# Optimization experiments

Measured on AMD Instinct MI355X. Metric: run time of the kernel, lower is better.

The kernel has to match this reference:

```python
import jax, jax.numpy as jnp
import numpy as np

N_NODES = 100000
N_EDGES = 3200000
NFEAT, NHID, NCLASS = 512, 256, 40


def spmm(edge_src, edge_dst, edge_w, h):
    # sparse adjacency @ h via gather + weighted segment-sum over destination nodes
    msgs = h[edge_src] * edge_w[:, None]          # [E, d]
    return jax.ops.segment_sum(msgs, edge_dst, num_segments=N_NODES)


def gcn_layer(h, W, b, edge_src, edge_dst, edge_w):
    support = h @ W                                # [N, d_out]
    return spmm(edge_src, edge_dst, edge_w, support) + b


def setup_inputs() -> dict:
    key = jax.random.key(0)
    ks = jax.random.split(key, 16)
    def w(k, shape, fan_in):
        return jax.random.normal(k, shape, dtype=jnp.float32) / np.sqrt(fan_in)
    inp = {
        'x': jax.random.normal(ks[0], (N_NODES, NFEAT), dtype=jnp.float32),
        'W1': w(ks[1], (NFEAT, NHID), NFEAT), 'b1': jnp.zeros((NHID,), jnp.float32),
        'W2': w(ks[2], (NHID, NHID), NHID),  'b2': jnp.zeros((NHID,), jnp.float32),
        'W3': w(ks[3], (NHID, NHID), NHID),  'b3': jnp.zeros((NHID,), jnp.float32),
        'W4': w(ks[4], (NHID, NHID), NHID),  'b4': jnp.zeros((NHID,), jnp.float32),
        'W5': w(ks[5], (NHID, NHID), NHID),  'b5': jnp.zeros((NHID,), jnp.float32),
        'W6': w(ks[6], (NHID, NCLASS), NHID),'b6': jnp.zeros((NCLASS,), jnp.float32),
        'edge_w': jax.random.uniform(ks[7], (N_EDGES,), dtype=jnp.float32),
        'edge_src': jax.random.randint(ks[8], (N_EDGES,), 0, N_NODES, dtype=jnp.int32),
        'edge_dst': jax.random.randint(ks[9], (N_EDGES,), 0, N_NODES, dtype=jnp.int32),
    }
    return inp


def reference(x, W1, b1, W2, b2, W3, b3, W4, b4, W5, b5, W6, b6,
              edge_w, edge_src, edge_dst):
    # eval mode: dropout is identity
    h = jax.nn.relu(gcn_layer(x, W1, b1, edge_src, edge_dst, edge_w))
    h = jax.nn.relu(gcn_layer(h, W2, b2, edge_src, edge_dst, edge_w))
    h = jax.nn.relu(gcn_layer(h, W3, b3, edge_src, edge_dst, edge_w))
    h = jax.nn.relu(gcn_layer(h, W4, b4, edge_src, edge_dst, edge_w))
    h = jax.nn.relu(gcn_layer(h, W5, b5, edge_src, edge_dst, edge_w))
    h = gcn_layer(h, W6, b6, edge_src, edge_dst, edge_w)
    return jax.nn.log_softmax(h, axis=1)
```

## Files before the change

### kernel.cpp

```cpp
#include <hip/hip_runtime.h>
#include <hip/hip_bf16.h>

static const int NN = 100000;
static const int NE = 3200000;
static const int F0 = 512;
static const int FH = 256;
static const int NC = 40;

#define CHUNK_SHIFT 13
static const int NCH  = (NN + (1 << CHUNK_SHIFT) - 1) >> CHUNK_SHIFT;
static const int KEYS = NN * NCH;

#define NPB_SHIFT 8
static const int NPB = 1 << NPB_SHIFT;
static const int NB  = (NN + NPB - 1) >> NPB_SHIFT;
static const int KPB = NPB * NCH;
#define EPB_A 8192

typedef __attribute__((ext_vector_type(8))) short bf16x8;
typedef __attribute__((ext_vector_type(16))) float f32x16;

__device__ __forceinline__ float bf2f(unsigned short u) {
    union { unsigned int i; float f; } c; c.i = ((unsigned int)u) << 16; return c.f;
}
__device__ __forceinline__ unsigned short f2bf(float f) {
    __hip_bfloat16 h = __float2bfloat16(f);
    return *reinterpret_cast<unsigned short*>(&h);
}

__global__ __launch_bounds__(256) void hist_bucket(const int* __restrict__ dst,
                                                   int* __restrict__ bcount, int E) {
    __shared__ int h[NB];
    for (int i = threadIdx.x; i < NB; i += 256) h[i] = 0;
    __syncthreads();
    for (int e = blockIdx.x * 256 + threadIdx.x; e < E; e += gridDim.x * 256)
        atomicAdd(&h[dst[e] >> NPB_SHIFT], 1);
    __syncthreads();
    for (int i = threadIdx.x; i < NB; i += 256)
        if (h[i]) atomicAdd(&bcount[i], h[i]);
}

__global__ __launch_bounds__(512) void scan_buckets(const int* __restrict__ bcount,
                                                    int* __restrict__ bstart,
                                                    int* __restrict__ bcursor, int E) {
    __shared__ int t[512];
    int tid = threadIdx.x;
    int v = (tid < NB) ? bcount[tid] : 0;
    t[tid] = v;
    __syncthreads();
    for (int off = 1; off < 512; off <<= 1) {
        int u = (tid >= off) ? t[tid - off] : 0;
        __syncthreads();
        t[tid] += u;
        __syncthreads();
    }
    if (tid < NB) {
        int s = t[tid] - v;
        bstart[tid] = s;
        bcursor[tid] = s;
    }
    if (tid == 0) bstart[NB] = E;
}

__global__ __launch_bounds__(256) void bin_scatter(const int* __restrict__ src,
                                                   const int* __restrict__ dst,
                                                   const float* __restrict__ w,
                                                   int* __restrict__ bcursor,
                                                   uint2* __restrict__ binned, int E) {
    __shared__ int hist[NB];
    __shared__ int base[NB];
    int tid = threadIdx.x;
    int e0 = blockIdx.x * EPB_A;
    int e1 = e0 + EPB_A; if (e1 > E) e1 = E;
    for (int i = tid; i < NB; i += 256) hist[i] = 0;
    __syncthreads();
    for (int e = e0 + tid; e < e1; e += 256)
        atomicAdd(&hist[dst[e] >> NPB_SHIFT], 1);
    __syncthreads();
    for (int i = tid; i < NB; i += 256) {
        int c = hist[i];
        base[i] = c ? atomicAdd(&bcursor[i], c) : 0;
        hist[i] = 0;
    }
    __syncthreads();
    for (int e = e0 + tid; e < e1; e += 256) {
        int d = dst[e];
        int b = d >> NPB_SHIFT;
        int off = atomicAdd(&hist[b], 1);
        unsigned int wq = (unsigned int)rintf(w[e] * 32767.f);
        unsigned int packed = ((unsigned int)src[e] << 15) | wq;
        binned[base[b] + off] = make_uint2(packed, (unsigned int)d);
    }
}

__global__ __launch_bounds__(256) void bin_sort(const uint2* __restrict__ binned,
                                                const int* __restrict__ bstart,
                                                int* __restrict__ keyStart,
                                                unsigned int* __restrict__ ev, int E) {
    __shared__ int hist[KPB];
    __shared__ int part[256];
    int b = blockIdx.x;
    int tid = threadIdx.x;
    int nodeLo = b << NPB_SHIFT;
    int eLo = bstart[b], eHi = bstart[b + 1];

    for (int i = tid; i < KPB; i += 256) hist[i] = 0;
    __syncthreads();
    for (int e = eLo + tid; e < eHi; e += 256) {
        uint2 r = binned[e];
        int lkey = ((int)r.y - nodeLo) * NCH + (int)(r.x >> (15 + CHUNK_SHIFT));
        atomicAdd(&hist[lkey], 1);
    }
    __syncthreads();

    int k0 = tid * NCH;
    int loc[NCH];
    int s = 0;
    #pragma unroll
    for (int j = 0; j < NCH; j++) { int c = hist[k0 + j]; loc[j] = s; s += c; }
    part[tid] = s;
    __syncthreads();
    for (int off = 1; off < 256; off <<= 1) {
        int u = (tid >= off) ? part[tid - off] : 0;
        __syncthreads();
        part[tid] += u;
        __syncthreads();
    }
    int excl = (tid > 0) ? part[tid - 1] : 0;
    __syncthreads();
    #pragma unroll
    for (int j = 0; j < NCH; j++) hist[k0 + j] = loc[j] + excl;
    __syncthreads();

    int keyBase = nodeLo * NCH;
    int kMax = KEYS - keyBase; if (kMax > KPB) kMax = KPB;
    for (int i = tid; i < kMax; i += 256) keyStart[keyBase + i] = eLo + hist[i];
    if (b == gridDim.x - 1 && tid == 0) keyStart[KEYS] = E;
    __syncthreads();

    for (int e = eLo + tid; e < eHi; e += 256) {
        uint2 r = binned[e];
        int lkey = ((int)r.y - nodeLo) * NCH + (int)(r.x >> (15 + CHUNK_SHIFT));
        int pos = eLo + atomicAdd(&hist[lkey], 1);
        ev[pos] = r.x;
    }
}

__global__ void transpose_cast(const float* __restrict__ W, unsigned short* __restrict__ Wt,
                               int K, int N) {
    int idx = blockIdx.x * 256 + threadIdx.x;
    if (idx >= K * N) return;
    int n = idx / K;
    int k = idx - n * K;
    Wt[idx] = f2bf(W[(size_t)k * N + n]);
}

template <int A_IS_F32>
__global__ __launch_bounds__(256) void gemm_mfma_q(const void* __restrict__ Aptr,
                                                   const unsigned short* __restrict__ Wt,
                                                   unsigned char* __restrict__ Cq,
                                                   float* __restrict__ scales,
                                                   int M, int K) {
    __shared__ short Bs[256][40];
    const int tid = threadIdx.x;
    const int w = tid >> 6;
    const int l = tid & 63;
    const int m0 = blockIdx.x * 128 + w * 32;
    const int lrow = l & 31;
    const int lgrp = l >> 5;
    int row_a = m0 + lrow;
    if (row_a > M - 1) row_a = M - 1;

    f32x16 acc[8] = {};

    for (int kk = 0; kk < K; kk += 32) {
        __syncthreads();
        {
            const unsigned short* srcp = Wt + (size_t)tid * K + kk;
            #pragma unroll
            for (int i = 0; i < 4; i++) {
                *reinterpret_cast<bf16x8*>(&Bs[tid][i * 8]) =
                    *reinterpret_cast<const bf16x8*>(srcp + i * 8);
            }
        }
        __syncthreads();

        #pragma unroll
        for (int s = 0; s < 2; s++) {
            const int kbase = kk + s * 16 + lgrp * 8;
            bf16x8 a;
            if (A_IS_F32) {
                const float* p = (const float*)Aptr + (size_t)row_a * K + kbase;
                #pragma unroll
                for (int j = 0; j < 8; j++) a[j] = (short)f2bf(p[j]);
            } else {
                const unsigned short* p = (const unsigned short*)Aptr + (size_t)row_a * K + kbase;
                a = *reinterpret_cast<const bf16x8*>(p);
            }
            #pragma unroll
            for (int nt = 0; nt < 8; nt++) {
                bf16x8 b = *reinterpret_cast<const bf16x8*>(&Bs[nt * 32 + lrow][s * 16 + lgrp * 8]);
                acc[nt] = __builtin_amdgcn_mfma_f32_32x32x16_bf16(a, b, acc[nt], 0, 0, 0);
            }
        }
    }

    #pragma unroll
    for (int r = 0; r < 16; r++) {
        float vm = 0.f;
        #pragma unroll
        for (int nt = 0; nt < 8; nt++) vm = fmaxf(vm, fabsf(acc[nt][r]));
        #pragma unroll
        for (int off = 1; off < 32; off <<= 1) vm = fmaxf(vm, __shfl_xor(vm, off));
        int row = m0 + (r & 3) + 8 * (r >> 2) + 4 * lgrp;
        float inv = (vm > 0.f) ? 127.f / vm : 0.f;
        if (row < M) {
            if (lrow == 0) scales[row] = vm * (1.f / 127.f);
            #pragma unroll
            for (int nt = 0; nt < 8; nt++) {
                int q = (int)rintf(acc[nt][r] * inv) + 128;
                Cq[(size_t)row * 256 + nt * 32 + lrow] = (unsigned char)q;
            }
        }
    }
}

__global__ __launch_bounds__(256) void spmm_kernel(const unsigned char* __restrict__ supq,
                                                   const float* __restrict__ scales,
                                                   const unsigned int* __restrict__ ev,
                                                   const int* __restrict__ keyStart,
                                                   const float* __restrict__ bias,
                                                   unsigned short* __restrict__ out,
                                                   int M, int do_relu) {
    int node = blockIdx.x * 4 + (threadIdx.x >> 6);
    int l = threadIdx.x & 63;
    if (node >= M) return;
    const int g = l >> 4;
    const int lane16 = l & 15;
    const int boff = lane16 * 16;
    const int kb = node * NCH;
    int e0 = keyStart[kb], e1 = keyStart[kb + NCH];

    float acc[16] = {};
    float sw = 0.f;
    int e = e0 + g;
    for (; e + 4 < e1; e += 8) {
        unsigned int m0 = ev[e], m1 = ev[e + 4];
        int s0 = m0 >> 15, s1 = m1 >> 15;
        float w0 = (float)(m0 & 0x7fffu) * scales[s0];
        float w1 = (float)(m1 & 0x7fffu) * scales[s1];
        uint4 r0 = *(const uint4*)(supq + (size_t)s0 * 256 + boff);
        uint4 r1 = *(const uint4*)(supq + (size_t)s1 * 256 + boff);
        sw += w0 + w1;
        const unsigned int rr0[4] = {r0.x, r0.y, r0.z, r0.w};
        const unsigned int rr1[4] = {r1.x, r1.y, r1.z, r1.w};
        #pragma unroll
        for (int q = 0; q < 4; q++) {
            #pragma unroll
            for (int j = 0; j < 4; j++) {
                acc[q * 4 + j] += w0 * (float)((rr0[q] >> (8 * j)) & 0xffu)
                                + w1 * (float)((rr1[q] >> (8 * j)) & 0xffu);
            }
        }
    }
    for (; e < e1; e += 4) {
        unsigned int m0 = ev[e];
        int s0 = m0 >> 15;
        float w0 = (float)(m0 & 0x7fffu) * scales[s0];
        uint4 r0 = *(const uint4*)(supq + (size_t)s0 * 256 + boff);
        sw += w0;
        const unsigned int rr0[4] = {r0.x, r0.y, r0.z, r0.w};
        #pragma unroll
        for (int q = 0; q < 4; q++) {
            #pragma unroll
            for (int j = 0; j < 4; j++)
                acc[q * 4 + j] += w0 * (float)((rr0[q] >> (8 * j)) & 0xffu);
        }
    }

    #pragma unroll
    for (int j = 0; j < 16; j++) {
        acc[j] += __shfl_xor(acc[j], 16);
        acc[j] += __shfl_xor(acc[j], 32);
    }
    sw += __shfl_xor(sw, 16);
    sw += __shfl_xor(sw, 32);

    if (g == 0) {
        const float* bp = bias + boff;
        bf16x8 o0, o1;
        #pragma unroll
        for (int j = 0; j < 8; j++) {
            float v = (acc[j] - 128.f * sw) * (1.f / 32767.f) + bp[j];
            if (do_relu) v = fmaxf(v, 0.f);
            o0[j] = (short)f2bf(v);
        }
        #pragma unroll
        for (int j = 0; j < 8; j++) {
            float v = (acc[8 + j] - 128.f * sw) * (1.f / 32767.f) + bp[8 + j];
            if (do_relu) v = fmaxf(v, 0.f);
            o1[j] = (short)f2bf(v);
        }
        *reinterpret_cast<bf16x8*>(out + (size_t)node * 256 + boff) = o0;
        *reinterpret_cast<bf16x8*>(out + (size_t)node * 256 + boff + 8) = o1;
    }
}

__global__ __launch_bounds__(256) void gemm6_mfma(const unsigned short* __restrict__ h,
                                                  const unsigned short* __restrict__ Wt6,
                                                  unsigned short* __restrict__ sup6, int M) {
    __shared__ short Bs[64][40];
    const int tid = threadIdx.x;
    const int w = tid >> 6;
    const int l = tid & 63;
    const int m0 = blockIdx.x * 128 + w * 32;
    const int lrow = l & 31;
    const int lgrp = l >> 5;
    int row_a = m0 + lrow;
    if (row_a > M - 1) row_a = M - 1;

    f32x16 acc[2] = {};

    for (int kk = 0; kk < 256; kk += 32) {
        __syncthreads();
        {
            int r = tid >> 2, part = tid & 3;
            bf16x8 v = {};
            if (r < NC) v = *(const bf16x8*)(Wt6 + (size_t)r * 256 + kk + part * 8);
            *reinterpret_cast<bf16x8*>(&Bs[r][part * 8]) = v;
        }
        __syncthreads();

        #pragma unroll
        for (int s = 0; s < 2; s++) {
            const unsigned short* pa = h + (size_t)row_a * 256 + kk + s * 16 + lgrp * 8;
            bf16x8 a = *(const bf16x8*)pa;
            #pragma unroll
            for (int nt = 0; nt < 2; nt++) {
                bf16x8 b = *(const bf16x8*)(&Bs[nt * 32 + lrow][s * 16 + lgrp * 8]);
                acc[nt] = __builtin_amdgcn_mfma_f32_32x32x16_bf16(a, b, acc[nt], 0, 0, 0);
            }
        }
    }

    #pragma unroll
    for (int nt = 0; nt < 2; nt++) {
        #pragma unroll
        for (int r = 0; r < 16; r++) {
            int row = m0 + (r & 3) + 8 * (r >> 2) + 4 * lgrp;
            int col = nt * 32 + lrow;
            if (row < M && col < NC) sup6[(size_t)row * NC + col] = f2bf(acc[nt][r]);
        }
    }
}

__global__ __launch_bounds__(256) void spmm6_lsm(const unsigned short* __restrict__ sup6,
                                                 const unsigned int* __restrict__ ev,
                                                 const int* __restrict__ keyStart,
                                                 const float* __restrict__ b6,
                                                 float* __restrict__ out, int M) {
    int node = blockIdx.x * 4 + (threadIdx.x >> 6);
    int l = threadIdx.x & 63;
    if (node >= M) return;
    const int kb = node * NCH;
    int e0 = keyStart[kb], e1 = keyStart[kb + NCH];
    float acc = 0.f;
    bool active = (l < NC);
    int cix = active ? l : 0;
    int e = e0;
    for (; e + 4 <= e1; e += 4) {
        unsigned int m0 = ev[e], m1 = ev[e + 1], m2 = ev[e + 2], m3 = ev[e + 3];
        float v0 = bf2f(sup6[(size_t)(m0 >> 15) * NC + cix]);
        float v1 = bf2f(sup6[(size_t)(m1 >> 15) * NC + cix]);
        float v2 = bf2f(sup6[(size_t)(m2 >> 15) * NC + cix]);
        float v3 = bf2f(sup6[(size_t)(m3 >> 15) * NC + cix]);
        acc += (float)(m0 & 0x7fffu) * v0 + (float)(m1 & 0x7fffu) * v1
             + (float)(m2 & 0x7fffu) * v2 + (float)(m3 & 0x7fffu) * v3;
    }
    for (; e < e1; e++) {
        unsigned int m0 = ev[e];
        acc += (float)(m0 & 0x7fffu) * bf2f(sup6[(size_t)(m0 >> 15) * NC + cix]);
    }
    acc *= (1.f / 32767.f);

    float x = active ? (acc + b6[l]) : -__builtin_inff();
    float mx = x;
    #pragma unroll
    for (int off = 32; off > 0; off >>= 1) mx = fmaxf(mx, __shfl_xor(mx, off));
    float ex = active ? __expf(x - mx) : 0.f;
    float sm = ex;
    #pragma unroll
    for (int off = 32; off > 0; off >>= 1) sm += __shfl_xor(sm, off);
    if (active) out[(size_t)node * NC + l] = x - mx - __logf(sm);
}

extern "C" void kernel_launch(void* const* d_in, const int* in_sizes, int n_in,
                              void* d_out, int out_size, void* d_ws, size_t ws_size,
                              hipStream_t stream) {
    const float* x  = (const float*)d_in[0];
    const float* W1 = (const float*)d_in[1];  const float* b1 = (const float*)d_in[2];
    const float* W2 = (const float*)d_in[3];  const float* b2 = (const float*)d_in[4];
    const float* W3 = (const float*)d_in[5];  const float* b3 = (const float*)d_in[6];
    const float* W4 = (const float*)d_in[7];  const float* b4 = (const float*)d_in[8];
    const float* W5 = (const float*)d_in[9];  const float* b5 = (const float*)d_in[10];
    const float* W6 = (const float*)d_in[11]; const float* b6 = (const float*)d_in[12];
    const float* edge_w  = (const float*)d_in[13];
    const int* edge_src  = (const int*)d_in[14];
    const int* edge_dst  = (const int*)d_in[15];

    char* p = (char*)d_ws;
    auto alloc = [&](size_t bytes) -> char* {
        char* r = p;
        p += (bytes + 255) & ~(size_t)255;
        return r;
    };
    unsigned short* h_a = (unsigned short*)alloc((size_t)NN * FH * 2);
    unsigned short* h_b = (unsigned short*)alloc((size_t)NN * FH * 2);
    unsigned char* supq = (unsigned char*)alloc((size_t)NN * 256);
    float* scales       = (float*)alloc((size_t)NN * 4);
    unsigned int* ev    = (unsigned int*)alloc((size_t)NE * 4);
    int* keyStart  = (int*)alloc((size_t)(KEYS + 1) * 4);
    int* bcount    = (int*)alloc((size_t)NB * 4);
    int* bstart    = (int*)alloc((size_t)(NB + 1) * 4);
    int* bcursor   = (int*)alloc((size_t)NB * 4);
    unsigned short* Wt1 = (unsigned short*)alloc((size_t)FH * F0 * 2);
    unsigned short* Wt2 = (unsigned short*)alloc((size_t)FH * FH * 2);
    unsigned short* Wt3 = (unsigned short*)alloc((size_t)FH * FH * 2);
    unsigned short* Wt4 = (unsigned short*)alloc((size_t)FH * FH * 2);
    unsigned short* Wt5 = (unsigned short*)alloc((size_t)FH * FH * 2);
    unsigned short* Wt6 = (unsigned short*)alloc((size_t)NC * FH * 2);
    unsigned short* sup6 = h_b;
    uint2* binned = (uint2*)h_b;

    hipMemsetAsync(bcount, 0, (size_t)NB * 4, stream);
    hist_bucket<<<512, 256, 0, stream>>>(edge_dst, bcount, NE);
    scan_buckets<<<1, 512, 0, stream>>>(bcount, bstart, bcursor, NE);
    bin_scatter<<<(NE + EPB_A - 1) / EPB_A, 256, 0, stream>>>(edge_src, edge_dst, edge_w,
                                                              bcursor, binned, NE);
    bin_sort<<<NB, 256, 0, stream>>>(binned, bstart, keyStart, ev, NE);

    transpose_cast<<<(F0 * FH + 255) / 256, 256, 0, stream>>>(W1, Wt1, F0, FH);
    transpose_cast<<<(FH * FH + 255) / 256, 256, 0, stream>>>(W2, Wt2, FH, FH);
    transpose_cast<<<(FH * FH + 255) / 256, 256, 0, stream>>>(W3, Wt3, FH, FH);
    transpose_cast<<<(FH * FH + 255) / 256, 256, 0, stream>>>(W4, Wt4, FH, FH);
    transpose_cast<<<(FH * FH + 255) / 256, 256, 0, stream>>>(W5, Wt5, FH, FH);
    transpose_cast<<<(FH * NC + 255) / 256, 256, 0, stream>>>(W6, Wt6, FH, NC);

    const int gemmGrid = (NN + 127) / 128;
    const int rowGrid  = (NN + 3) / 4;

    gemm_mfma_q<1><<<gemmGrid, 256, 0, stream>>>(x, Wt1, supq, scales, NN, F0);
    spmm_kernel<<<rowGrid, 256, 0, stream>>>(supq, scales, ev, keyStart, b1, h_a, NN, 1);
    gemm_mfma_q<0><<<gemmGrid, 256, 0, stream>>>(h_a, Wt2, supq, scales, NN, FH);
    spmm_kernel<<<rowGrid, 256, 0, stream>>>(supq, scales, ev, keyStart, b2, h_b, NN, 1);
    gemm_mfma_q<0><<<gemmGrid, 256, 0, stream>>>(h_b, Wt3, supq, scales, NN, FH);
    spmm_kernel<<<rowGrid, 256, 0, stream>>>(supq, scales, ev, keyStart, b3, h_a, NN, 1);
    gemm_mfma_q<0><<<gemmGrid, 256, 0, stream>>>(h_a, Wt4, supq, scales, NN, FH);
    spmm_kernel<<<rowGrid, 256, 0, stream>>>(supq, scales, ev, keyStart, b4, h_b, NN, 1);
    gemm_mfma_q<0><<<gemmGrid, 256, 0, stream>>>(h_b, Wt5, supq, scales, NN, FH);
    spmm_kernel<<<rowGrid, 256, 0, stream>>>(supq, scales, ev, keyStart, b5, h_a, NN, 1);
    gemm6_mfma<<<gemmGrid, 256, 0, stream>>>(h_a, Wt6, sup6, NN);
    spmm6_lsm<<<rowGrid, 256, 0, stream>>>(sup6, ev, keyStart, b6, (float*)d_out, NN);
}
```

Baseline: 1.301 ms.

## Stage full 256-wide K tile of weights in LDS with 512-thread GEMM blocks

```diff
diff --git a/kernel.cpp b/kernel.cpp
--- a/kernel.cpp
+++ b/kernel.cpp
@@ -156,16 +156,16 @@
 }
 
 template <int A_IS_F32>
-__global__ __launch_bounds__(256) void gemm_mfma_q(const void* __restrict__ Aptr,
-                                                   const unsigned short* __restrict__ Wt,
-                                                   unsigned char* __restrict__ Cq,
-                                                   float* __restrict__ scales,
-                                                   int M, int K) {
-    __shared__ short Bs[256][40];
+__global__ __launch_bounds__(512, 2) void gemm_mfma_q(const void* __restrict__ Aptr,
+                                                      const unsigned short* __restrict__ Wt,
+                                                      unsigned char* __restrict__ Cq,
+                                                      float* __restrict__ scales,
+                                                      int M, int K) {
+    __shared__ short Bs[65536];
     const int tid = threadIdx.x;
     const int w = tid >> 6;
     const int l = tid & 63;
-    const int m0 = blockIdx.x * 128 + w * 32;
+    const int m0 = blockIdx.x * 256 + w * 32;
     const int lrow = l & 31;
     const int lgrp = l >> 5;
     int row_a = m0 + lrow;
@@ -173,34 +173,42 @@
 
     f32x16 acc[8] = {};
 
-    for (int kk = 0; kk < K; kk += 32) {
-        __syncthreads();
-        {
-            const unsigned short* srcp = Wt + (size_t)tid * K + kk;
+    for (int kt = 0; kt < K; kt += 256) {
+        if (kt) __syncthreads();
+        #pragma unroll
+        for (int it = 0; it < 16; ++it) {
+            int fid = it * 512 + tid;
+            int c = fid & 255;
+            int f = fid >> 8;
+            bf16x8 v = *reinterpret_cast<const bf16x8*>(Wt + (size_t)c * K + kt + f * 8);
+            *reinterpret_cast<bf16x8*>(&Bs[((f << 8) + c) * 8]) = v;
+        }
+        __syncthreads();
+
+        for (int kk = 0; kk < 256; kk += 32) {
+            bf16x8 a0, a1;
+            if (A_IS_F32) {
+                const float* p0 = (const float*)Aptr + (size_t)row_a * K + kt + kk + lgrp * 8;
+                const float* p1 = p0 + 16;
+                #pragma unroll
+                for (int j = 0; j < 8; j++) a0[j] = (short)f2bf(p0[j]);
+                #pragma unroll
+                for (int j = 0; j < 8; j++) a1[j] = (short)f2bf(p1[j]);
+            } else {
+                const unsigned short* p = (const unsigned short*)Aptr + (size_t)row_a * K + kt + kk + lgrp * 8;
+                a0 = *reinterpret_cast<const bf16x8*>(p);
+                a1 = *reinterpret_cast<const bf16x8*>(p + 16);
+            }
+            const int fbase = kk >> 3;
             #pragma unroll
-            for (int i = 0; i < 4; i++) {
-                *reinterpret_cast<bf16x8*>(&Bs[tid][i * 8]) =
-                    *reinterpret_cast<const bf16x8*>(srcp + i * 8);
-            }
-        }
-        __syncthreads();
-
-        #pragma unroll
-        for (int s = 0; s < 2; s++) {
-            const int kbase = kk + s * 16 + lgrp * 8;
-            bf16x8 a;
-            if (A_IS_F32) {
-                const float* p = (const float*)Aptr + (size_t)row_a * K + kbase;
+            for (int s = 0; s < 2; s++) {
+                const short* bp = &Bs[((fbase + s * 2 + lgrp) << 8) * 8];
+                bf16x8 a = s ? a1 : a0;
                 #pragma unroll
-                for (int j = 0; j < 8; j++) a[j] = (short)f2bf(p[j]);
-            } else {
-                const unsigned short* p = (const unsigned short*)Aptr + (size_t)row_a * K + kbase;
-                a = *reinterpret_cast<const bf16x8*>(p);
-            }
-            #pragma unroll
-            for (int nt = 0; nt < 8; nt++) {
-                bf16x8 b = *reinterpret_cast<const bf16x8*>(&Bs[nt * 32 + lrow][s * 16 + lgrp * 8]);
-                acc[nt] = __builtin_amdgcn_mfma_f32_32x32x16_bf16(a, b, acc[nt], 0, 0, 0);
+                for (int nt = 0; nt < 8; nt++) {
+                    bf16x8 b = *reinterpret_cast<const bf16x8*>(bp + (nt * 32 + lrow) * 8);
+                    acc[nt] = __builtin_amdgcn_mfma_f32_32x32x16_bf16(a, b, acc[nt], 0, 0, 0);
+                }
             }
         }
     }
@@ -446,19 +454,20 @@
     transpose_cast<<<(FH * FH + 255) / 256, 256, 0, stream>>>(W5, Wt5, FH, FH);
     transpose_cast<<<(FH * NC + 255) / 256, 256, 0, stream>>>(W6, Wt6, FH, NC);
 
-    const int gemmGrid = (NN + 127) / 128;
+    const int gemmGrid = (NN + 255) / 256;
+    const int g6Grid   = (NN + 127) / 128;
     const int rowGrid  = (NN + 3) / 4;
 
-    gemm_mfma_q<1><<<gemmGrid, 256, 0, stream>>>(x, Wt1, supq, scales, NN, F0);
+    gemm_mfma_q<1><<<gemmGrid, 512, 0, stream>>>(x, Wt1, supq, scales, NN, F0);
     spmm_kernel<<<rowGrid, 256, 0, stream>>>(supq, scales, ev, keyStart, b1, h_a, NN, 1);
-    gemm_mfma_q<0><<<gemmGrid, 256, 0, stream>>>(h_a, Wt2, supq, scales, NN, FH);
+    gemm_mfma_q<0><<<gemmGrid, 512, 0, stream>>>(h_a, Wt2, supq, scales, NN, FH);
     spmm_kernel<<<rowGrid, 256, 0, stream>>>(supq, scales, ev, keyStart, b2, h_b, NN, 1);
-    gemm_mfma_q<0><<<gemmGrid, 256, 0, stream>>>(h_b, Wt3, supq, scales, NN, FH);
+    gemm_mfma_q<0><<<gemmGrid, 512, 0, stream>>>(h_b, Wt3, supq, scales, NN, FH);
     spmm_kernel<<<rowGrid, 256, 0, stream>>>(supq, scales, ev, keyStart, b3, h_a, NN, 1);
-    gemm_mfma_q<0><<<gemmGrid, 256, 0, stream>>>(h_a, Wt4, supq, scales, NN, FH);
+    gemm_mfma_q<0><<<gemmGrid, 512, 0, stream>>>(h_a, Wt4, supq, scales, NN, FH);
     spmm_kernel<<<rowGrid, 256, 0, stream>>>(supq, scales, ev, keyStart, b4, h_b, NN, 1);
-    gemm_mfma_q<0><<<gemmGrid, 256, 0, stream>>>(h_b, Wt5, supq, scales, NN, FH);
+    gemm_mfma_q<0><<<gemmGrid, 512, 0, stream>>>(h_b, Wt5, supq, scales, NN, FH);
     spmm_kernel<<<rowGrid, 256, 0, stream>>>(supq, scales, ev, keyStart, b5, h_a, NN, 1);
-    gemm6_mfma<<<gemmGrid, 256, 0, stream>>>(h_a, Wt6, sup6, NN);
+    gemm6_mfma<<<g6Grid, 256, 0, stream>>>(h_a, Wt6, sup6, NN);
     spmm6_lsm<<<rowGrid, 256, 0, stream>>>(sup6, ev, keyStart, b6, (float*)d_out, NN);
 }
```

Result: faster. 1.152 ms (-11.5%).
